# Kernel tuning notes

Measured on AMD Instinct MI355X. Metric: run time of the kernel, lower is better.

Reference implementation:

```python
import jax, jax.numpy as jnp
import numpy as np

B, N, IN_FT, OUT_FT = 256, 512, 64, 64


def setup_inputs() -> dict:
    key = jax.random.key(0)
    k1, k2, k3 = jax.random.split(key, 3)
    seq = jax.random.normal(k1, (B, N, IN_FT), dtype=jnp.float32)
    adj = jax.random.uniform(k2, (B, N, N), dtype=jnp.float32)
    # Xavier-uniform linear weight [out_ft, in_ft]
    limit = float(np.sqrt(6.0 / (IN_FT + OUT_FT)))
    W = jax.random.uniform(k3, (OUT_FT, IN_FT), dtype=jnp.float32, minval=-limit, maxval=limit)
    bias = jnp.zeros((OUT_FT,), dtype=jnp.float32)  # bias.data.fill_(0.0)
    alpha = jnp.asarray(0.25, dtype=jnp.float32)    # PReLU default single param
    return {"seq": seq, "adj": adj, "W": W, "bias": bias, "alpha": alpha}


def reference(seq, adj, W, bias, alpha):
    # fc: seq @ W.T  -> [B, N, out_ft]
    seq_fts = jnp.einsum('bnf,of->bno', seq, W)
    # dense batched adjacency aggregation: adj @ seq_fts -> [B, N, out_ft]
    out = jnp.einsum('bnm,bmo->bno', adj, seq_fts)
    out = out + bias
    # PReLU with shared alpha
    return jnp.where(out >= 0, out, alpha * out)
```

## Files before the change

kernel.cpp:

```cpp
#include <hip/hip_runtime.h>
#include <hip/hip_bf16.h>


#define BATCH 256
#define NTOK  512
#define INF   64
#define OUTF  64

typedef __attribute__((ext_vector_type(8))) __bf16 bf16x8;
typedef __attribute__((ext_vector_type(4))) __bf16 bf16x4;
typedef __attribute__((ext_vector_type(4))) float  f32x4;

typedef const __attribute__((address_space(1))) char GChar;
typedef __attribute__((address_space(3))) char LChar;

__device__ __forceinline__ bf16x8 load_cvt8(const float* __restrict__ p) {
    float4 lo = *(const float4*)p;
    float4 hi = *(const float4*)(p + 4);
    bf16x8 r;
    r[0] = (__bf16)lo.x; r[1] = (__bf16)lo.y; r[2] = (__bf16)lo.z; r[3] = (__bf16)lo.w;
    r[4] = (__bf16)hi.x; r[5] = (__bf16)hi.y; r[6] = (__bf16)hi.z; r[7] = (__bf16)hi.w;
    return r;
}

__device__ __forceinline__ bf16x8 pack8(float4 lo, float4 hi) {
    bf16x8 r;
    r[0] = (__bf16)lo.x; r[1] = (__bf16)lo.y; r[2] = (__bf16)lo.z; r[3] = (__bf16)lo.w;
    r[4] = (__bf16)hi.x; r[5] = (__bf16)hi.y; r[6] = (__bf16)hi.z; r[7] = (__bf16)hi.w;
    return r;
}

__global__ __launch_bounds__(512, 2) void GCN_fused_kernel(
        const float* __restrict__ seq, const float* __restrict__ adj,
        const float* __restrict__ W, const float* __restrict__ bias,
        const float* __restrict__ alpha_p, float* __restrict__ out) {
    __shared__ float smem[32768];

    int b    = blockIdx.x;
    int tid  = threadIdx.x;
    int wave = tid >> 6;
    int lane = tid & 63;
    int row16 = lane & 15;
    int g     = lane >> 4;
    int c     = wave & 3;
    int mt    = wave >> 2;
    int rs    = row16 & 7;

    __bf16* sft = (__bf16*)smem;
    float* buf0 = smem + 16384;
    float* buf1 = smem;

    const float* gadj = adj + (size_t)b * NTOK * NTOK;

#define STAGE(dstf, rbase) do {                                                \
    _Pragma("unroll")                                                          \
    for (int i_ = 0; i_ < 8; ++i_) {                                           \
        int idx_  = wave * 8 + i_;                                             \
        int row_  = idx_ >> 1;                                                 \
        int half_ = idx_ & 1;                                                  \
        __builtin_amdgcn_global_load_lds(                                      \
            (GChar*)(gadj + (size_t)((rbase) + row_) * NTOK + half_ * 256      \
                     + (lane ^ (row_ & 7)) * 4),                               \
            (LChar*)((dstf) + idx_ * 256), 16, 0, 0);                          \
    }                                                                          \
} while (0)

    STAGE(buf0, 0);

    {
        int mb = wave * 64;
        bf16x8 wf[4][2];
#pragma unroll
        for (int nt = 0; nt < 4; ++nt)
#pragma unroll
            for (int ks = 0; ks < 2; ++ks)
                wf[nt][ks] = load_cvt8(W + (size_t)(nt * 16 + row16) * INF + ks * 32 + g * 8);

#pragma unroll
        for (int mt2 = 0; mt2 < 4; ++mt2) {
            f32x4 pa[4] = {};
#pragma unroll
            for (int ks = 0; ks < 2; ++ks) {
                bf16x8 af = load_cvt8(seq + ((size_t)b * NTOK + mb + mt2 * 16 + row16) * INF + ks * 32 + g * 8);
#pragma unroll
                for (int nt = 0; nt < 4; ++nt)
                    pa[nt] = __builtin_amdgcn_mfma_f32_16x16x32_bf16(af, wf[nt][ks], pa[nt], 0, 0, 0);
            }
#pragma unroll
            for (int nt = 0; nt < 4; ++nt) {
                int o    = nt * 16 + row16;
                int ktok = mb + mt2 * 16 + g * 4;
                int sw   = (ktok >> 3) ^ (o & 7);
                bf16x4 v;
                v[0] = (__bf16)pa[nt][0]; v[1] = (__bf16)pa[nt][1];
                v[2] = (__bf16)pa[nt][2]; v[3] = (__bf16)pa[nt][3];
                *(bf16x4*)((char*)sft + (size_t)o * 1024 + sw * 16 + (ktok & 7) * 2) = v;
            }
        }
    }
    int orow     = c * 16 + row16;
    float bv     = bias[orow];
    float alphav = alpha_p[0];
    __syncthreads();

    bf16x8 bbr[16];
#pragma unroll
    for (int t = 0; t < 16; ++t) {
        int sw = ((t << 2) + g) ^ rs;
        bbr[t] = *(const bf16x8*)((const char*)sft + (size_t)orow * 1024 + sw * 16);
    }
    __syncthreads();

#pragma unroll 1
    for (int it = 0; it < 16; ++it) {
        float* cur = (it & 1) ? buf1 : buf0;
        float* nxt = (it & 1) ? buf0 : buf1;

        if (it > 0) {
            __builtin_amdgcn_sched_barrier(0);
            __builtin_amdgcn_s_barrier();
            __builtin_amdgcn_sched_barrier(0);
        }
        if (it < 15) STAGE(nxt, (it + 1) * 32);
        __builtin_amdgcn_sched_barrier(0);
        if (it == 0)       asm volatile("s_waitcnt vmcnt(8)"  ::: "memory");
        else if (it < 15)  asm volatile("s_waitcnt vmcnt(12)" ::: "memory");
        else               asm volatile("s_waitcnt vmcnt(4)"  ::: "memory");
        __builtin_amdgcn_sched_barrier(0);
        __builtin_amdgcn_s_barrier();
        __builtin_amdgcn_sched_barrier(0);

        f32x4 acc;
        acc[0] = bv; acc[1] = bv; acc[2] = bv; acc[3] = bv;
        int rowb = (mt * 16 + row16) * 512;
#pragma unroll
        for (int ks = 0; ks < 16; ++ks) {
            int s0 = (ks * 8 + g * 2) ^ rs;
            float4 f0 = *(const float4*)(cur + rowb + s0 * 4);
            float4 f1 = *(const float4*)(cur + rowb + (s0 ^ 1) * 4);
            bf16x8 a = pack8(f0, f1);
            acc = __builtin_amdgcn_mfma_f32_16x16x32_bf16(a, bbr[ks], acc, 0, 0, 0);
        }

        int m = it * 32 + mt * 16 + g * 4;
        float* op = out + ((size_t)b * NTOK + m) * OUTF + orow;
#pragma unroll
        for (int j = 0; j < 4; ++j) {
            float v = acc[j];
            op[(size_t)j * OUTF] = (v >= 0.f) ? v : alphav * v;
        }
    }
#undef STAGE
}

extern "C" void kernel_launch(void* const* d_in, const int* in_sizes, int n_in,
                              void* d_out, int out_size, void* d_ws, size_t ws_size,
                              hipStream_t stream) {
    const float* seq   = (const float*)d_in[0];
    const float* adj   = (const float*)d_in[1];
    const float* W     = (const float*)d_in[2];
    const float* bias  = (const float*)d_in[3];
    const float* alpha = (const float*)d_in[4];
    float* out = (float*)d_out;

    GCN_fused_kernel<<<dim3(BATCH), dim3(512), 0, stream>>>(seq, adj, W, bias, alpha, out);
}
```

Measured before the change: 72.09 us.

## Give each wave private adjacency row panels to drop block-wide barriers

Switches to 256 threads per block, with each wave owning 128 output rows. Each wave streams its own 16x128 adjacency chunks into a private double buffer, so the per-iteration s_barrier disappears and only wave-local vmcnt waits remain. Every wave now computes all four output column tiles and reads the B fragments from LDS on each MFMA instead of keeping them in registers. In exchange there are half as many waves per block, a 64 KB shared-memory footprint that limits occupancy, more LDS traffic for the B operand, and smaller 8 KB chunks in flight per wave.

```diff
diff --git a/kernel.cpp b/kernel.cpp
--- a/kernel.cpp
+++ b/kernel.cpp
@@ -30,7 +30,7 @@
     return r;
 }
 
-__global__ __launch_bounds__(512, 2) void GCN_fused_kernel(
+__global__ __launch_bounds__(256, 1) void GCN_fused_kernel(
         const float* __restrict__ seq, const float* __restrict__ adj,
         const float* __restrict__ W, const float* __restrict__ bias,
         const float* __restrict__ alpha_p, float* __restrict__ out) {
@@ -42,33 +42,33 @@
     int lane = tid & 63;
     int row16 = lane & 15;
     int g     = lane >> 4;
-    int c     = wave & 3;
-    int mt    = wave >> 2;
     int rs    = row16 & 7;
 
     __bf16* sft = (__bf16*)smem;
-    float* buf0 = smem + 16384;
-    float* buf1 = smem;
+    float* bufA = smem + 16384 + wave * 4096;
+    float* bufB = bufA + 2048;
 
     const float* gadj = adj + (size_t)b * NTOK * NTOK;
 
-#define STAGE(dstf, rbase) do {                                                \
+#define STAGE(dstf, CH) do {                                                   \
+    int rb_ = wave * 128 + ((CH) >> 2) * 16;                                   \
+    int kb_ = ((CH) & 3) * 128;                                                \
     _Pragma("unroll")                                                          \
     for (int i_ = 0; i_ < 8; ++i_) {                                           \
-        int idx_  = wave * 8 + i_;                                             \
-        int row_  = idx_ >> 1;                                                 \
-        int half_ = idx_ & 1;                                                  \
+        int rl_ = 2 * i_ + (lane >> 5);                                        \
+        int sl_ = (lane & 31) ^ (rl_ & 7);                                     \
         __builtin_amdgcn_global_load_lds(                                      \
-            (GChar*)(gadj + (size_t)((rbase) + row_) * NTOK + half_ * 256      \
-                     + (lane ^ (row_ & 7)) * 4),                               \
-            (LChar*)((dstf) + idx_ * 256), 16, 0, 0);                          \
+            (GChar*)(gadj + (size_t)(rb_ + rl_) * NTOK + kb_ + sl_ * 4),       \
+            (LChar*)((dstf) + i_ * 256), 16, 0, 0);                            \
     }                                                                          \
 } while (0)
 
-    STAGE(buf0, 0);
+    STAGE(bufA, 0);
+    STAGE(bufB, 1);
+    __builtin_amdgcn_sched_barrier(0);
 
     {
-        int mb = wave * 64;
+        int mb = wave * 128;
         bf16x8 wf[4][2];
 #pragma unroll
         for (int nt = 0; nt < 4; ++nt)
@@ -77,7 +77,7 @@
                 wf[nt][ks] = load_cvt8(W + (size_t)(nt * 16 + row16) * INF + ks * 32 + g * 8);
 
 #pragma unroll
-        for (int mt2 = 0; mt2 < 4; ++mt2) {
+        for (int mt2 = 0; mt2 < 8; ++mt2) {
             f32x4 pa[4] = {};
 #pragma unroll
             for (int ks = 0; ks < 2; ++ks) {
@@ -98,57 +98,62 @@
             }
         }
     }
-    int orow     = c * 16 + row16;
-    float bv     = bias[orow];
+    float bvv[4];
+#pragma unroll
+    for (int ct = 0; ct < 4; ++ct) bvv[ct] = bias[ct * 16 + row16];
     float alphav = alpha_p[0];
     __syncthreads();
 
-    bf16x8 bbr[16];
+    f32x4 acc[4];
 #pragma unroll
-    for (int t = 0; t < 16; ++t) {
-        int sw = ((t << 2) + g) ^ rs;
-        bbr[t] = *(const bf16x8*)((const char*)sft + (size_t)orow * 1024 + sw * 16);
+    for (int ct = 0; ct < 4; ++ct) {
+        acc[ct][0] = bvv[ct]; acc[ct][1] = bvv[ct];
+        acc[ct][2] = bvv[ct]; acc[ct][3] = bvv[ct];
     }
-    __syncthreads();
 
-#pragma unroll 1
-    for (int it = 0; it < 16; ++it) {
-        float* cur = (it & 1) ? buf1 : buf0;
-        float* nxt = (it & 1) ? buf0 : buf1;
+#pragma unroll
+    for (int ch = 0; ch < 32; ++ch) {
+        float* cur = (ch & 1) ? bufB : bufA;
 
-        if (it > 0) {
-            __builtin_amdgcn_sched_barrier(0);
-            __builtin_amdgcn_s_barrier();
-            __builtin_amdgcn_sched_barrier(0);
-        }
-        if (it < 15) STAGE(nxt, (it + 1) * 32);
-        __builtin_amdgcn_sched_barrier(0);
-        if (it == 0)       asm volatile("s_waitcnt vmcnt(8)"  ::: "memory");
-        else if (it < 15)  asm volatile("s_waitcnt vmcnt(12)" ::: "memory");
-        else               asm volatile("s_waitcnt vmcnt(4)"  ::: "memory");
-        __builtin_amdgcn_sched_barrier(0);
-        __builtin_amdgcn_s_barrier();
+        if (ch == 0)                        asm volatile("s_waitcnt vmcnt(8)"  ::: "memory");
+        else if (ch == 31)                  asm volatile("s_waitcnt vmcnt(0)"  ::: "memory");
+        else if ((ch & 3) == 0)             asm volatile("s_waitcnt vmcnt(24)" ::: "memory");
+        else                                asm volatile("s_waitcnt vmcnt(8)"  ::: "memory");
         __builtin_amdgcn_sched_barrier(0);
 
-        f32x4 acc;
-        acc[0] = bv; acc[1] = bv; acc[2] = bv; acc[3] = bv;
-        int rowb = (mt * 16 + row16) * 512;
 #pragma unroll
-        for (int ks = 0; ks < 16; ++ks) {
-            int s0 = (ks * 8 + g * 2) ^ rs;
-            float4 f0 = *(const float4*)(cur + rowb + s0 * 4);
-            float4 f1 = *(const float4*)(cur + rowb + (s0 ^ 1) * 4);
+        for (int t = 0; t < 4; ++t) {
+            int sw = (t * 8 + g * 2) ^ rs;
+            float4 f0 = *(const float4*)(cur + row16 * 128 + sw * 4);
+            float4 f1 = *(const float4*)(cur + row16 * 128 + (sw ^ 1) * 4);
             bf16x8 a = pack8(f0, f1);
-            acc = __builtin_amdgcn_mfma_f32_16x16x32_bf16(a, bbr[ks], acc, 0, 0, 0);
+#pragma unroll
+            for (int ct = 0; ct < 4; ++ct) {
+                int slot = (((ch & 3) * 4 + t) * 4 + g) ^ rs;
+                bf16x8 bb = *(const bf16x8*)((const char*)sft
+                              + (size_t)(ct * 16 + row16) * 1024 + slot * 16);
+                acc[ct] = __builtin_amdgcn_mfma_f32_16x16x32_bf16(a, bb, acc[ct], 0, 0, 0);
+            }
         }
+        __builtin_amdgcn_sched_barrier(0);
 
-        int m = it * 32 + mt * 16 + g * 4;
-        float* op = out + ((size_t)b * NTOK + m) * OUTF + orow;
+        if ((ch & 3) == 3) {
+            int rp = ch >> 2;
 #pragma unroll
-        for (int j = 0; j < 4; ++j) {
-            float v = acc[j];
-            op[(size_t)j * OUTF] = (v >= 0.f) ? v : alphav * v;
+            for (int ct = 0; ct < 4; ++ct) {
+#pragma unroll
+                for (int j = 0; j < 4; ++j) {
+                    float v = acc[ct][j];
+                    out[((size_t)b * NTOK + wave * 128 + rp * 16 + g * 4 + j) * OUTF
+                        + ct * 16 + row16] = (v >= 0.f) ? v : alphav * v;
+                }
+                acc[ct][0] = bvv[ct]; acc[ct][1] = bvv[ct];
+                acc[ct][2] = bvv[ct]; acc[ct][3] = bvv[ct];
+            }
         }
+        __builtin_amdgcn_sched_barrier(0);
+        if (ch + 2 <= 31) STAGE(((ch & 1) ? bufB : bufA), ch + 2);
+        __builtin_amdgcn_sched_barrier(0);
     }
 #undef STAGE
 }
@@ -163,5 +168,5 @@
     const float* alpha = (const float*)d_in[4];
     float* out = (float*)d_out;
 
-    GCN_fused_kernel<<<dim3(BATCH), dim3(512), 0, stream>>>(seq, adj, W, bias, alpha, out);
+    GCN_fused_kernel<<<dim3(BATCH), dim3(256), 0, stream>>>(seq, adj, W, bias, alpha, out);
 }
```

Result: slower. 73.97 us (+2.6%).

## Retile adjacency aggregation into 64-row groups split by K-halves with 2 N-tiles per wave

Applied to the files above, without the earlier changes.

Waves now own a 16-row by 32-column output tile (two MFMA accumulators) instead of 16x16, so each adjacency A-fragment read from LDS and converted to bf16 feeds two MFMAs. The adjacency stream is restaged as 64-row groups split into two K-halves that alternate between the two LDS buffers, giving 8 outer iterations with two compute phases each. Outputs are shuffled across lanes with ds_bpermute so each lane writes a contiguous float2. In exchange, each wave holds twice as many B fragments in registers, and the bpermute adds cross-lane traffic.

```diff
diff --git a/kernel.cpp b/kernel.cpp
--- a/kernel.cpp
+++ b/kernel.cpp
@@ -42,8 +42,8 @@
     int lane = tid & 63;
     int row16 = lane & 15;
     int g     = lane >> 4;
-    int c     = wave & 3;
-    int mt    = wave >> 2;
+    int mt    = wave >> 1;
+    int c2    = wave & 1;
     int rs    = row16 & 7;
 
     __bf16* sft = (__bf16*)smem;
@@ -52,20 +52,19 @@
 
     const float* gadj = adj + (size_t)b * NTOK * NTOK;
 
-#define STAGE(dstf, rbase) do {                                                \
+#define STAGE(dstf, RG, KH) do {                                               \
     _Pragma("unroll")                                                          \
     for (int i_ = 0; i_ < 8; ++i_) {                                           \
-        int idx_  = wave * 8 + i_;                                             \
-        int row_  = idx_ >> 1;                                                 \
-        int half_ = idx_ & 1;                                                  \
+        int idx_ = wave * 8 + i_;                                              \
         __builtin_amdgcn_global_load_lds(                                      \
-            (GChar*)(gadj + (size_t)((rbase) + row_) * NTOK + half_ * 256      \
-                     + (lane ^ (row_ & 7)) * 4),                               \
+            (GChar*)(gadj + (size_t)((RG) * 64 + idx_) * NTOK + (KH) * 256     \
+                     + ((lane ^ (idx_ & 7)) << 2)),                            \
             (LChar*)((dstf) + idx_ * 256), 16, 0, 0);                          \
     }                                                                          \
 } while (0)
 
-    STAGE(buf0, 0);
+    STAGE(buf0, 0, 0);
+    __builtin_amdgcn_sched_barrier(0);
 
     {
         int mb = wave * 64;
@@ -98,59 +97,99 @@
             }
         }
     }
-    int orow     = c * 16 + row16;
-    float bv     = bias[orow];
+    float bv2[2];
+#pragma unroll
+    for (int ti = 0; ti < 2; ++ti) bv2[ti] = bias[c2 * 32 + ti * 16 + row16];
     float alphav = alpha_p[0];
     __syncthreads();
 
-    bf16x8 bbr[16];
-#pragma unroll
-    for (int t = 0; t < 16; ++t) {
-        int sw = ((t << 2) + g) ^ rs;
-        bbr[t] = *(const bf16x8*)((const char*)sft + (size_t)orow * 1024 + sw * 16);
+    bf16x8 bbr2[16][2];
+#pragma unroll
+    for (int t = 0; t < 16; ++t)
+#pragma unroll
+        for (int ti = 0; ti < 2; ++ti) {
+            int o  = c2 * 32 + ti * 16 + row16;
+            int sw = ((t << 2) + g) ^ rs;
+            bbr2[t][ti] = *(const bf16x8*)((const char*)sft + (size_t)o * 1024 + sw * 16);
+        }
+    __syncthreads();
+
+    f32x4 acc2[2];
+#pragma unroll
+    for (int ti = 0; ti < 2; ++ti) {
+        acc2[ti][0] = bv2[ti]; acc2[ti][1] = bv2[ti];
+        acc2[ti][2] = bv2[ti]; acc2[ti][3] = bv2[ti];
     }
-    __syncthreads();
+
+#define COMPUTE(curf, KH) do {                                                 \
+    int rowb_ = (mt * 16 + row16) * 256;                                       \
+    _Pragma("unroll")                                                          \
+    for (int tt_ = 0; tt_ < 8; ++tt_) {                                        \
+        int s0_ = ((tt_ * 8 + g * 2) ^ rs);                                    \
+        float4 f0_ = *(const float4*)((curf) + rowb_ + s0_ * 4);               \
+        float4 f1_ = *(const float4*)((curf) + rowb_ + (s0_ ^ 1) * 4);         \
+        bf16x8 a_ = pack8(f0_, f1_);                                           \
+        acc2[0] = __builtin_amdgcn_mfma_f32_16x16x32_bf16(a_, bbr2[(KH) * 8 + tt_][0], acc2[0], 0, 0, 0); \
+        acc2[1] = __builtin_amdgcn_mfma_f32_16x16x32_bf16(a_, bbr2[(KH) * 8 + tt_][1], acc2[1], 0, 0, 0); \
+    }                                                                          \
+} while (0)
 
 #pragma unroll 1
-    for (int it = 0; it < 16; ++it) {
-        float* cur = (it & 1) ? buf1 : buf0;
-        float* nxt = (it & 1) ? buf0 : buf1;
-
-        if (it > 0) {
+    for (int rg = 0; rg < 8; ++rg) {
+        if (rg > 0) {
             __builtin_amdgcn_sched_barrier(0);
             __builtin_amdgcn_s_barrier();
             __builtin_amdgcn_sched_barrier(0);
         }
-        if (it < 15) STAGE(nxt, (it + 1) * 32);
-        __builtin_amdgcn_sched_barrier(0);
-        if (it == 0)       asm volatile("s_waitcnt vmcnt(8)"  ::: "memory");
-        else if (it < 15)  asm volatile("s_waitcnt vmcnt(12)" ::: "memory");
-        else               asm volatile("s_waitcnt vmcnt(4)"  ::: "memory");
+        STAGE(buf1, rg, 1);
+        __builtin_amdgcn_sched_barrier(0);
+        if (rg == 0) asm volatile("s_waitcnt vmcnt(8)"  ::: "memory");
+        else         asm volatile("s_waitcnt vmcnt(12)" ::: "memory");
         __builtin_amdgcn_sched_barrier(0);
         __builtin_amdgcn_s_barrier();
         __builtin_amdgcn_sched_barrier(0);
-
-        f32x4 acc;
-        acc[0] = bv; acc[1] = bv; acc[2] = bv; acc[3] = bv;
-        int rowb = (mt * 16 + row16) * 512;
-#pragma unroll
-        for (int ks = 0; ks < 16; ++ks) {
-            int s0 = (ks * 8 + g * 2) ^ rs;
-            float4 f0 = *(const float4*)(cur + rowb + s0 * 4);
-            float4 f1 = *(const float4*)(cur + rowb + (s0 ^ 1) * 4);
-            bf16x8 a = pack8(f0, f1);
-            acc = __builtin_amdgcn_mfma_f32_16x16x32_bf16(a, bbr[ks], acc, 0, 0, 0);
-        }
-
-        int m = it * 32 + mt * 16 + g * 4;
-        float* op = out + ((size_t)b * NTOK + m) * OUTF + orow;
-#pragma unroll
-        for (int j = 0; j < 4; ++j) {
-            float v = acc[j];
-            op[(size_t)j * OUTF] = (v >= 0.f) ? v : alphav * v;
+        COMPUTE(buf0, 0);
+
+        __builtin_amdgcn_sched_barrier(0);
+        __builtin_amdgcn_s_barrier();
+        __builtin_amdgcn_sched_barrier(0);
+        if (rg < 7) STAGE(buf0, rg + 1, 0);
+        __builtin_amdgcn_sched_barrier(0);
+        if (rg < 7) asm volatile("s_waitcnt vmcnt(8)" ::: "memory");
+        else        asm volatile("s_waitcnt vmcnt(0)" ::: "memory");
+        __builtin_amdgcn_sched_barrier(0);
+        __builtin_amdgcn_s_barrier();
+        __builtin_amdgcn_sched_barrier(0);
+        COMPUTE(buf1, 1);
+
+        {
+            float p0[4], p1[4];
+#pragma unroll
+            for (int j = 0; j < 4; ++j) {
+                float v0 = acc2[0][j]; p0[j] = (v0 >= 0.f) ? v0 : alphav * v0;
+                float v1 = acc2[1][j]; p1[j] = (v1 >= 0.f) ? v1 : alphav * v1;
+            }
+            int addrA = (g * 16 + ((2 * row16) & 15)) << 2;
+            int addrB = (g * 16 + ((2 * row16 + 1) & 15)) << 2;
+            bool loSel = (row16 < 8);
+#pragma unroll
+            for (int j = 0; j < 4; ++j) {
+                int a0 = __builtin_amdgcn_ds_bpermute(addrA, __float_as_int(p0[j]));
+                int a1 = __builtin_amdgcn_ds_bpermute(addrA, __float_as_int(p1[j]));
+                int b0 = __builtin_amdgcn_ds_bpermute(addrB, __float_as_int(p0[j]));
+                int b1 = __builtin_amdgcn_ds_bpermute(addrB, __float_as_int(p1[j]));
+                float lo = __int_as_float(loSel ? a0 : a1);
+                float hi = __int_as_float(loSel ? b0 : b1);
+                float2 st = make_float2(lo, hi);
+                *(float2*)(out + ((size_t)b * NTOK + rg * 64 + mt * 16 + g * 4 + j) * OUTF
+                           + c2 * 32 + 2 * row16) = st;
+                acc2[0][j] = bv2[0];
+                acc2[1][j] = bv2[1];
+            }
         }
     }
 #undef STAGE
+#undef COMPUTE
 }
 
 extern "C" void kernel_launch(void* const* d_in, const int* in_sizes, int n_in,
```

After: 68.66 us. 1.05x faster.
